# Kernel optimization log

Hardware: AMD Instinct MI355X
Metric: run time of the kernel (lower is better)

The kernel has to match this reference:

```python
import jax, jax.numpy as jnp
import numpy as np

N, D, B, C, T, TOD = 8192, 32, 2, 8, 12, 288
PARAM_SCALE = 0.3  # keep relu+softmax logits well-conditioned (original uses plain randn init)


def setup_inputs() -> dict:
    key = jax.random.key(0)
    k0, k1, k2, k3, k4 = jax.random.split(key, 5)
    return {
        "x": jax.random.normal(k0, (B, C, N, T), dtype=jnp.float32),
        "nodevec1": PARAM_SCALE * jax.random.normal(k1, (N, D), dtype=jnp.float32),
        "nodevec2": PARAM_SCALE * jax.random.normal(k2, (N, D), dtype=jnp.float32),
        "timevec": PARAM_SCALE * jax.random.normal(k3, (TOD, D), dtype=jnp.float32),
        "k": PARAM_SCALE * jax.random.normal(k4, (D, D, D), dtype=jnp.float32),
        "time_ind": 100,
    }


def reference(x, nodevec1, nodevec2, timevec, k, time_ind):
    # Dynamic Tucker-decomposition adjacency (SpatialGraphConv.forward, eval mode -> dropout is identity)
    tv = timevec[time_ind]                             # [D]   time_vec
    core = jnp.einsum('d,def->ef', tv, k)              # [D,D] adp1 (squeezed)
    # adp2/adp3 chain: (nodevec1 @ core) @ nodevec2.T  -> [N,N]
    adp = jnp.einsum('ne,ef->nf', nodevec1, core)      # [N,D]
    adp = jnp.einsum('nf,mf->nm', adp, nodevec2)       # [N,N]
    adp = jax.nn.softmax(jax.nn.relu(adp), axis=-1)    # row-softmax over neighbors
    # NConv: neighbor aggregation  'bcnt,nm->bcmt'
    return jnp.einsum('bcnt,nm->bcmt', x, adp)
```

## Files before the change

### kernel.cpp

```cpp
#include <hip/hip_runtime.h>
#include <hip/hip_bf16.h>


#define NN 8192
#define DD 32
#define TT 12
#define NSPLIT 8
#define CHUNK 1024
#define ESTR 72

typedef __attribute__((ext_vector_type(8))) short bf16x8;
typedef __attribute__((ext_vector_type(4))) short bf16x4;
typedef __attribute__((ext_vector_type(4))) float f32x4;

static __device__ __forceinline__ unsigned short f2bf(float f) {
  unsigned int u = __float_as_uint(f);
  u = (u + 0x7FFFu + ((u >> 16) & 1u)) >> 16;
  return (unsigned short)u;
}

static __device__ __forceinline__ float fexp2(float x) {
#if __has_builtin(__builtin_amdgcn_exp2f)
  return __builtin_amdgcn_exp2f(x);
#else
  return __builtin_exp2f(x);
#endif
}

__global__ __launch_bounds__(256) void k_prep(const float* __restrict__ nv1,
                                              const float* __restrict__ nv2,
                                              const float* __restrict__ timevec,
                                              const float* __restrict__ kk,
                                              const int* __restrict__ tind,
                                              unsigned short* __restrict__ t1b,
                                              unsigned short* __restrict__ nv2b,
                                              float* __restrict__ sums) {
  __shared__ float cs[1024];
  const int tid = threadIdx.x;
  if (tid < 128) sums[blockIdx.x * 128 + tid] = 0.f;
  const float* tv = timevec + (size_t)tind[0] * DD;
  for (int idx = tid; idx < 1024; idx += 256) {
    float acc = 0.f;
#pragma unroll
    for (int d = 0; d < DD; ++d) acc += tv[d] * kk[d * 1024 + idx];
    cs[idx] = acc;
  }
  __syncthreads();
  const int nbase = blockIdx.x * 128;
  const int f = tid & 31, sub = tid >> 5;
#pragma unroll 4
  for (int it = 0; it < 16; ++it) {
    const int n = nbase + it * 8 + sub;
    const float* nr = nv1 + (size_t)n * DD;
    float acc = 0.f;
#pragma unroll
    for (int e = 0; e < DD; ++e) acc += nr[e] * cs[e * DD + f];
    t1b[(size_t)n * DD + f] = f2bf(acc * 1.4426950408889634f);
  }
#pragma unroll 4
  for (int it = 0; it < 16; ++it) {
    const int idx = nbase * DD + it * 256 + tid;
    nv2b[idx] = f2bf(nv2[idx]);
  }
}

__global__ __launch_bounds__(256) void k_stats(const unsigned short* __restrict__ t1b,
                                               const unsigned short* __restrict__ nv2b,
                                               float* __restrict__ sums) {
  const int tid = threadIdx.x;
  const int w = tid >> 6, lane = tid & 63, q = lane >> 4, i16 = lane & 15;
  const int nbase = blockIdx.x * 64 + w * 16;
  bf16x8 a = *(const bf16x8*)(t1b + (size_t)(nbase + i16) * DD + q * 8);
  const f32x4 z4 = {0.f, 0.f, 0.f, 0.f};
  float s[4] = {0.f, 0.f, 0.f, 0.f};
  const int m0 = blockIdx.y * 1024;
  for (int mt = m0; mt < m0 + 1024; mt += 64) {
#pragma unroll
    for (int u = 0; u < 4; ++u) {
      bf16x8 b = *(const bf16x8*)(nv2b + (size_t)(mt + u * 16 + i16) * DD + q * 8);
      f32x4 d = __builtin_amdgcn_mfma_f32_16x16x32_bf16(a, b, z4, 0, 0, 0);
#pragma unroll
      for (int r = 0; r < 4; ++r) s[r] += fexp2(fmaxf(d[r], 0.f));
    }
  }
#pragma unroll
  for (int r = 0; r < 4; ++r)
    for (int off = 1; off < 16; off <<= 1) s[r] += __shfl_xor(s[r], off, 64);
  if (i16 == 0) {
#pragma unroll
    for (int r = 0; r < 4; ++r) atomicAdd(&sums[nbase + q * 4 + r], s[r]);
  }
}

__global__ __launch_bounds__(256) void k_y(const float* __restrict__ x,
                                           const float* __restrict__ sums,
                                           unsigned short* __restrict__ yT) {
  __shared__ float xs[3072];
  const int tid = threadIdx.x;
  const int n0 = blockIdx.x * 256;
  const int bc = blockIdx.y;
  const float* xp = x + (size_t)bc * NN * TT + (size_t)n0 * TT;
#pragma unroll
  for (int j = 0; j < 12; ++j) xs[j * 256 + tid] = xp[j * 256 + tid];
  __syncthreads();
  const float rinv = 1.0f / sums[n0 + tid];
#pragma unroll
  for (int t = 0; t < 12; ++t)
    yT[(size_t)(bc * TT + t) * NN + n0 + tid] = f2bf(xs[tid * 12 + t] * rinv);
}

__global__ __launch_bounds__(256, 4) void k_mega(const unsigned short* __restrict__ t1b,
                                                 const unsigned short* __restrict__ nv2b,
                                                 const unsigned short* __restrict__ yT,
                                                 float* __restrict__ part) {
  const int tid = threadIdx.x;
  const int w = tid >> 6, lane = tid & 63, q = lane >> 4, i16 = lane & 15;
  const int mb = blockIdx.x * 64;
  const int nt0 = blockIdx.y * CHUNK;

  __shared__ unsigned short Ew[2][64][ESTR];

  const bf16x8 bg = *(const bf16x8*)(nv2b + (size_t)(mb + w * 16 + i16) * DD + q * 8);
  const int rowm = w * 16 + i16;

  const f32x4 z4 = {0.f, 0.f, 0.f, 0.f};
  f32x4 acc[3][4];
#pragma unroll
  for (int c = 0; c < 3; ++c)
#pragma unroll
    for (int ms = 0; ms < 4; ++ms) acc[c][ms] = (f32x4){0.f, 0.f, 0.f, 0.f};

#pragma unroll
  for (int s = 0; s < 4; ++s) {
    bf16x8 at = *(const bf16x8*)(t1b + (size_t)(nt0 + s * 16 + i16) * DD + q * 8);
    f32x4 d = __builtin_amdgcn_mfma_f32_16x16x32_bf16(at, bg, z4, 0, 0, 0);
    bf16x4 e;
#pragma unroll
    for (int r = 0; r < 4; ++r) e[r] = (short)f2bf(fexp2(fmaxf(d[r], 0.f)));
    *(bf16x4*)&Ew[0][rowm][s * 16 + q * 4] = e;
  }
  __syncthreads();

  int p = 0;
  for (int st = 0; st < 16; ++st, p ^= 1) {
    const int nt = nt0 + st * 64;
    const bool more = (st < 15);

    bf16x8 atn[4];
    if (more) {
#pragma unroll
      for (int s = 0; s < 4; ++s)
        atn[s] = *(const bf16x8*)(t1b + (size_t)(nt + 64 + s * 16 + i16) * DD + q * 8);
    }

    bf16x8 yfr[3], efr[4];
#pragma unroll
    for (int c = 0; c < 3; ++c)
      yfr[c] = *(const bf16x8*)(yT + (size_t)((w * 3 + c) * 16 + i16) * NN + nt + q * 8);
#pragma unroll
    for (int ms = 0; ms < 4; ++ms)
      efr[ms] = *(const bf16x8*)&Ew[p][ms * 16 + i16][q * 8];

    f32x4 d0, d1;
    if (more) {
      d0 = __builtin_amdgcn_mfma_f32_16x16x32_bf16(atn[0], bg, z4, 0, 0, 0);
      d1 = __builtin_amdgcn_mfma_f32_16x16x32_bf16(atn[1], bg, z4, 0, 0, 0);
    }

#pragma unroll
    for (int c = 0; c < 3; ++c)
#pragma unroll
      for (int ms = 0; ms < 4; ++ms)
        acc[c][ms] = __builtin_amdgcn_mfma_f32_16x16x32_bf16(yfr[c], efr[ms], acc[c][ms], 0, 0, 0);

    if (more) {
      bf16x4 e0, e1;
#pragma unroll
      for (int r = 0; r < 4; ++r) {
        e0[r] = (short)f2bf(fexp2(fmaxf(d0[r], 0.f)));
        e1[r] = (short)f2bf(fexp2(fmaxf(d1[r], 0.f)));
      }
      *(bf16x4*)&Ew[p ^ 1][rowm][q * 4] = e0;
      *(bf16x4*)&Ew[p ^ 1][rowm][16 + q * 4] = e1;
      f32x4 d2 = __builtin_amdgcn_mfma_f32_16x16x32_bf16(atn[2], bg, z4, 0, 0, 0);
      f32x4 d3 = __builtin_amdgcn_mfma_f32_16x16x32_bf16(atn[3], bg, z4, 0, 0, 0);
      bf16x4 e2, e3;
#pragma unroll
      for (int r = 0; r < 4; ++r) {
        e2[r] = (short)f2bf(fexp2(fmaxf(d2[r], 0.f)));
        e3[r] = (short)f2bf(fexp2(fmaxf(d3[r], 0.f)));
      }
      *(bf16x4*)&Ew[p ^ 1][rowm][32 + q * 4] = e2;
      *(bf16x4*)&Ew[p ^ 1][rowm][48 + q * 4] = e3;
    }

#pragma unroll
    for (int c = 0; c < 3; ++c)
      yfr[c] = *(const bf16x8*)(yT + (size_t)((w * 3 + c) * 16 + i16) * NN + nt + 32 + q * 8);
#pragma unroll
    for (int ms = 0; ms < 4; ++ms)
      efr[ms] = *(const bf16x8*)&Ew[p][ms * 16 + i16][32 + q * 8];
#pragma unroll
    for (int c = 0; c < 3; ++c)
#pragma unroll
      for (int ms = 0; ms < 4; ++ms)
        acc[c][ms] = __builtin_amdgcn_mfma_f32_16x16x32_bf16(yfr[c], efr[ms], acc[c][ms], 0, 0, 0);

    __syncthreads();
  }

  float* pp = part + (size_t)blockIdx.y * 192 * NN;
#pragma unroll
  for (int c = 0; c < 3; ++c)
#pragma unroll
    for (int ms = 0; ms < 4; ++ms) {
      const int colbase = (w * 3 + c) * 16 + q * 4;
      const int m = mb + ms * 16 + i16;
#pragma unroll
      for (int r = 0; r < 4; ++r)
        pp[(size_t)(colbase + r) * NN + m] = acc[c][ms][r];
    }
}

__global__ __launch_bounds__(256) void k_reduce(const float* __restrict__ part,
                                                float* __restrict__ out) {
  __shared__ float os[3072];
  const int tid = threadIdx.x;
  const int m0 = blockIdx.x * 256;
  const int bc = blockIdx.y;
#pragma unroll
  for (int t = 0; t < 12; ++t) {
    const int col = bc * TT + t;
    float s = 0.f;
#pragma unroll
    for (int nc = 0; nc < NSPLIT; ++nc)
      s += part[((size_t)nc * 192 + col) * NN + m0 + tid];
    os[tid * 12 + t] = s;
  }
  __syncthreads();
  float* op = out + (size_t)bc * NN * TT + (size_t)m0 * TT;
#pragma unroll
  for (int j = 0; j < 12; ++j) op[j * 256 + tid] = os[j * 256 + tid];
}

extern "C" void kernel_launch(void* const* d_in, const int* in_sizes, int n_in,
                              void* d_out, int out_size, void* d_ws, size_t ws_size,
                              hipStream_t stream) {
  const float* x = (const float*)d_in[0];
  const float* nv1 = (const float*)d_in[1];
  const float* nv2 = (const float*)d_in[2];
  const float* tv = (const float*)d_in[3];
  const float* kk = (const float*)d_in[4];
  const int* tind = (const int*)d_in[5];
  float* out = (float*)d_out;

  char* ws = (char*)d_ws;
  unsigned short* t1b  = (unsigned short*)(ws);
  unsigned short* nv2b = (unsigned short*)(ws + 524288);
  float* sums          = (float*)(ws + 1048576);
  unsigned short* yT   = (unsigned short*)(ws + 1081344);
  float* part          = (float*)(ws + 4227072);

  k_prep<<<64, 256, 0, stream>>>(nv1, nv2, tv, kk, tind, t1b, nv2b, sums);
  k_stats<<<dim3(128, 8), 256, 0, stream>>>(t1b, nv2b, sums);
  k_y<<<dim3(32, 16), 256, 0, stream>>>(x, sums, yT);
  k_mega<<<dim3(128, NSPLIT), 256, 0, stream>>>(t1b, nv2b, yT, part);
  k_reduce<<<dim3(32, 16), 256, 0, stream>>>(part, out);
}
```

Measured before the change: 178.8 us.

## Switch aggregation GEMM to 32x32x16 MFMA with two-stage t1 prefetch

The main aggregation GEMM moves from 16x16x32 to 32x32x16 bf16 MFMA, and the four waves are split as a 2x2 grid over output columns and m rows, which changes fragment loads and the output write pattern. Loads of the next t1 tile are issued two stages ahead and carried in registers, so the exp tile computation no longer waits on a global load issued in the same iteration. The larger MFMA tiles mean fewer LDS and global fragment loads per FLOP. The cost is more live registers, so launch bounds drop from 4 to 3 blocks per CU, which may reduce occupancy.

```diff
diff --git a/kernel.cpp b/kernel.cpp
--- a/kernel.cpp
+++ b/kernel.cpp
@@ -12,6 +12,7 @@
 typedef __attribute__((ext_vector_type(8))) short bf16x8;
 typedef __attribute__((ext_vector_type(4))) short bf16x4;
 typedef __attribute__((ext_vector_type(4))) float f32x4;
+typedef __attribute__((ext_vector_type(16))) float f32x16;
 
 static __device__ __forceinline__ unsigned short f2bf(float f) {
   unsigned int u = __float_as_uint(f);
@@ -109,12 +110,14 @@
     yT[(size_t)(bc * TT + t) * NN + n0 + tid] = f2bf(xs[tid * 12 + t] * rinv);
 }
 
-__global__ __launch_bounds__(256, 4) void k_mega(const unsigned short* __restrict__ t1b,
+__global__ __launch_bounds__(256, 3) void k_mega(const unsigned short* __restrict__ t1b,
                                                  const unsigned short* __restrict__ nv2b,
                                                  const unsigned short* __restrict__ yT,
                                                  float* __restrict__ part) {
   const int tid = threadIdx.x;
   const int w = tid >> 6, lane = tid & 63, q = lane >> 4, i16 = lane & 15;
+  const int h = lane >> 5, l31 = lane & 31;
+  const int wc = w & 1, wm = w >> 1;
   const int mb = blockIdx.x * 64;
   const int nt0 = blockIdx.y * CHUNK;
 
@@ -124,11 +127,11 @@
   const int rowm = w * 16 + i16;
 
   const f32x4 z4 = {0.f, 0.f, 0.f, 0.f};
-  f32x4 acc[3][4];
+  f32x16 acc[3];
 #pragma unroll
   for (int c = 0; c < 3; ++c)
 #pragma unroll
-    for (int ms = 0; ms < 4; ++ms) acc[c][ms] = (f32x4){0.f, 0.f, 0.f, 0.f};
+    for (int r = 0; r < 16; ++r) acc[c][r] = 0.f;
 
 #pragma unroll
   for (int s = 0; s < 4; ++s) {
@@ -139,6 +142,10 @@
     for (int r = 0; r < 4; ++r) e[r] = (short)f2bf(fexp2(fmaxf(d[r], 0.f)));
     *(bf16x4*)&Ew[0][rowm][s * 16 + q * 4] = e;
   }
+  bf16x8 atc[4];
+#pragma unroll
+  for (int s = 0; s < 4; ++s)
+    atc[s] = *(const bf16x8*)(t1b + (size_t)(nt0 + 64 + s * 16 + i16) * DD + q * 8);
   __syncthreads();
 
   int p = 0;
@@ -147,65 +154,47 @@
     const bool more = (st < 15);
 
     bf16x8 atn[4];
+    if (st < 14) {
+#pragma unroll
+      for (int s = 0; s < 4; ++s)
+        atn[s] = *(const bf16x8*)(t1b + (size_t)(nt + 128 + s * 16 + i16) * DD + q * 8);
+    }
+
+    bf16x8 yf[3][4];
+#pragma unroll
+    for (int c = 0; c < 3; ++c) {
+      const unsigned short* yp = yT + (size_t)((wc * 3 + c) * 32 + l31) * NN + nt + h * 8;
+#pragma unroll
+      for (int ks = 0; ks < 4; ++ks) yf[c][ks] = *(const bf16x8*)(yp + ks * 16);
+    }
+
+    bf16x8 ef[4];
+#pragma unroll
+    for (int ks = 0; ks < 4; ++ks)
+      ef[ks] = *(const bf16x8*)&Ew[p][wm * 32 + l31][ks * 16 + h * 8];
+
+    f32x4 dg[4];
     if (more) {
 #pragma unroll
       for (int s = 0; s < 4; ++s)
-        atn[s] = *(const bf16x8*)(t1b + (size_t)(nt + 64 + s * 16 + i16) * DD + q * 8);
-    }
-
-    bf16x8 yfr[3], efr[4];
-#pragma unroll
-    for (int c = 0; c < 3; ++c)
-      yfr[c] = *(const bf16x8*)(yT + (size_t)((w * 3 + c) * 16 + i16) * NN + nt + q * 8);
-#pragma unroll
-    for (int ms = 0; ms < 4; ++ms)
-      efr[ms] = *(const bf16x8*)&Ew[p][ms * 16 + i16][q * 8];
-
-    f32x4 d0, d1;
-    if (more) {
-      d0 = __builtin_amdgcn_mfma_f32_16x16x32_bf16(atn[0], bg, z4, 0, 0, 0);
-      d1 = __builtin_amdgcn_mfma_f32_16x16x32_bf16(atn[1], bg, z4, 0, 0, 0);
-    }
-
-#pragma unroll
-    for (int c = 0; c < 3; ++c)
-#pragma unroll
-      for (int ms = 0; ms < 4; ++ms)
-        acc[c][ms] = __builtin_amdgcn_mfma_f32_16x16x32_bf16(yfr[c], efr[ms], acc[c][ms], 0, 0, 0);
-
-    if (more) {
-      bf16x4 e0, e1;
-#pragma unroll
-      for (int r = 0; r < 4; ++r) {
-        e0[r] = (short)f2bf(fexp2(fmaxf(d0[r], 0.f)));
-        e1[r] = (short)f2bf(fexp2(fmaxf(d1[r], 0.f)));
+        dg[s] = __builtin_amdgcn_mfma_f32_16x16x32_bf16(atc[s], bg, z4, 0, 0, 0);
+#pragma unroll
+      for (int s = 0; s < 4; ++s) {
+        bf16x4 e;
+#pragma unroll
+        for (int r = 0; r < 4; ++r) e[r] = (short)f2bf(fexp2(fmaxf(dg[s][r], 0.f)));
+        *(bf16x4*)&Ew[p ^ 1][rowm][s * 16 + q * 4] = e;
       }
-      *(bf16x4*)&Ew[p ^ 1][rowm][q * 4] = e0;
-      *(bf16x4*)&Ew[p ^ 1][rowm][16 + q * 4] = e1;
-      f32x4 d2 = __builtin_amdgcn_mfma_f32_16x16x32_bf16(atn[2], bg, z4, 0, 0, 0);
-      f32x4 d3 = __builtin_amdgcn_mfma_f32_16x16x32_bf16(atn[3], bg, z4, 0, 0, 0);
-      bf16x4 e2, e3;
-#pragma unroll
-      for (int r = 0; r < 4; ++r) {
-        e2[r] = (short)f2bf(fexp2(fmaxf(d2[r], 0.f)));
-        e3[r] = (short)f2bf(fexp2(fmaxf(d3[r], 0.f)));
-      }
-      *(bf16x4*)&Ew[p ^ 1][rowm][32 + q * 4] = e2;
-      *(bf16x4*)&Ew[p ^ 1][rowm][48 + q * 4] = e3;
-    }
-
-#pragma unroll
-    for (int c = 0; c < 3; ++c)
-      yfr[c] = *(const bf16x8*)(yT + (size_t)((w * 3 + c) * 16 + i16) * NN + nt + 32 + q * 8);
-#pragma unroll
-    for (int ms = 0; ms < 4; ++ms)
-      efr[ms] = *(const bf16x8*)&Ew[p][ms * 16 + i16][32 + q * 8];
-#pragma unroll
-    for (int c = 0; c < 3; ++c)
-#pragma unroll
-      for (int ms = 0; ms < 4; ++ms)
-        acc[c][ms] = __builtin_amdgcn_mfma_f32_16x16x32_bf16(yfr[c], efr[ms], acc[c][ms], 0, 0, 0);
-
+    }
+
+#pragma unroll
+    for (int ks = 0; ks < 4; ++ks)
+#pragma unroll
+      for (int c = 0; c < 3; ++c)
+        acc[c] = __builtin_amdgcn_mfma_f32_32x32x16_bf16(yf[c][ks], ef[ks], acc[c], 0, 0, 0);
+
+#pragma unroll
+    for (int s = 0; s < 4; ++s) atc[s] = atn[s];
     __syncthreads();
   }
 
@@ -213,12 +202,9 @@
 #pragma unroll
   for (int c = 0; c < 3; ++c)
 #pragma unroll
-    for (int ms = 0; ms < 4; ++ms) {
-      const int colbase = (w * 3 + c) * 16 + q * 4;
-      const int m = mb + ms * 16 + i16;
-#pragma unroll
-      for (int r = 0; r < 4; ++r)
-        pp[(size_t)(colbase + r) * NN + m] = acc[c][ms][r];
+    for (int r = 0; r < 16; ++r) {
+      const int col = (wc * 3 + c) * 32 + (r & 3) + 8 * (r >> 2) + 4 * h;
+      pp[(size_t)col * NN + mb + wm * 32 + l31] = acc[c][r];
     }
 }
 
```

After: 217.8 us. 21.8% more time.

## Precompute whole exp-adjacency chunk into large LDS before the aggregation GEMM

Applied to the files above, without the earlier changes.

The main kernel now runs in two phases. First it computes the full 64x1024 tile of exp(relu(logits)) for its chunk and stores it in about 131 KB of dynamic LDS. Then it runs the aggregation MFMA loop with no per-step barriers or interleaved exp work, which removes the double-buffer synchronisation. The cost is that occupancy drops to one block per CU and the exp phase no longer overlaps with the GEMM. If the device reports too little shared memory per block, the launcher falls back to the old double-buffered kernel.

```diff
diff --git a/kernel.cpp b/kernel.cpp
--- a/kernel.cpp
+++ b/kernel.cpp
@@ -8,6 +8,8 @@
 #define NSPLIT 8
 #define CHUNK 1024
 #define ESTR 72
+#define ESTR2 1048
+#define MEGA_LDS (64 * ESTR2 * 2)
 
 typedef __attribute__((ext_vector_type(8))) short bf16x8;
 typedef __attribute__((ext_vector_type(4))) short bf16x4;
@@ -109,27 +111,101 @@
     yT[(size_t)(bc * TT + t) * NN + n0 + tid] = f2bf(xs[tid * 12 + t] * rinv);
 }
 
-__global__ __launch_bounds__(256, 4) void k_mega(const unsigned short* __restrict__ t1b,
+__global__ __launch_bounds__(256, 1) void k_mega(const unsigned short* __restrict__ t1b,
                                                  const unsigned short* __restrict__ nv2b,
                                                  const unsigned short* __restrict__ yT,
                                                  float* __restrict__ part) {
+  extern __shared__ unsigned short Et[];
   const int tid = threadIdx.x;
   const int w = tid >> 6, lane = tid & 63, q = lane >> 4, i16 = lane & 15;
   const int mb = blockIdx.x * 64;
   const int nt0 = blockIdx.y * CHUNK;
-
+  const f32x4 z4 = {0.f, 0.f, 0.f, 0.f};
+
+  {
+    const bf16x8 bg = *(const bf16x8*)(nv2b + (size_t)(mb + w * 16 + i16) * DD + q * 8);
+    unsigned short* erow = Et + (size_t)(w * 16 + i16) * ESTR2;
+    bf16x8 at[4], nx[4];
+#pragma unroll
+    for (int s = 0; s < 4; ++s)
+      at[s] = *(const bf16x8*)(t1b + (size_t)(nt0 + s * 16 + i16) * DD + q * 8);
+    for (int g = 0; g < 16; ++g) {
+      if (g < 15) {
+#pragma unroll
+        for (int s = 0; s < 4; ++s)
+          nx[s] = *(const bf16x8*)(t1b + (size_t)(nt0 + (g + 1) * 64 + s * 16 + i16) * DD + q * 8);
+      }
+#pragma unroll
+      for (int s = 0; s < 4; ++s) {
+        f32x4 d = __builtin_amdgcn_mfma_f32_16x16x32_bf16(at[s], bg, z4, 0, 0, 0);
+        bf16x4 e;
+#pragma unroll
+        for (int r = 0; r < 4; ++r) e[r] = (short)f2bf(fexp2(fmaxf(d[r], 0.f)));
+        *(bf16x4*)&erow[g * 64 + s * 16 + q * 4] = e;
+      }
+#pragma unroll
+      for (int s = 0; s < 4; ++s) at[s] = nx[s];
+    }
+  }
+  __syncthreads();
+
+  f32x4 acc[3][4];
+#pragma unroll
+  for (int c = 0; c < 3; ++c)
+#pragma unroll
+    for (int ms = 0; ms < 4; ++ms) acc[c][ms] = (f32x4){0.f, 0.f, 0.f, 0.f};
+
+  const unsigned short* yp[3];
+#pragma unroll
+  for (int c = 0; c < 3; ++c)
+    yp[c] = yT + (size_t)((w * 3 + c) * 16 + i16) * NN + nt0 + q * 8;
+
+#pragma unroll 2
+  for (int st = 0; st < 32; ++st) {
+    const int nb = st * 32;
+    bf16x8 yfr[3], efr[4];
+#pragma unroll
+    for (int c = 0; c < 3; ++c) yfr[c] = *(const bf16x8*)(yp[c] + nb);
+#pragma unroll
+    for (int ms = 0; ms < 4; ++ms)
+      efr[ms] = *(const bf16x8*)&Et[(size_t)(ms * 16 + i16) * ESTR2 + nb + q * 8];
+#pragma unroll
+    for (int c = 0; c < 3; ++c)
+#pragma unroll
+      for (int ms = 0; ms < 4; ++ms)
+        acc[c][ms] = __builtin_amdgcn_mfma_f32_16x16x32_bf16(yfr[c], efr[ms], acc[c][ms], 0, 0, 0);
+  }
+
+  float* pp = part + (size_t)blockIdx.y * 192 * NN;
+#pragma unroll
+  for (int c = 0; c < 3; ++c)
+#pragma unroll
+    for (int ms = 0; ms < 4; ++ms) {
+      const int colbase = (w * 3 + c) * 16 + q * 4;
+      const int m = mb + ms * 16 + i16;
+#pragma unroll
+      for (int r = 0; r < 4; ++r)
+        pp[(size_t)(colbase + r) * NN + m] = acc[c][ms][r];
+    }
+}
+
+__global__ __launch_bounds__(256, 4) void k_mega_fb(const unsigned short* __restrict__ t1b,
+                                                    const unsigned short* __restrict__ nv2b,
+                                                    const unsigned short* __restrict__ yT,
+                                                    float* __restrict__ part) {
+  const int tid = threadIdx.x;
+  const int w = tid >> 6, lane = tid & 63, q = lane >> 4, i16 = lane & 15;
+  const int mb = blockIdx.x * 64;
+  const int nt0 = blockIdx.y * CHUNK;
   __shared__ unsigned short Ew[2][64][ESTR];
-
   const bf16x8 bg = *(const bf16x8*)(nv2b + (size_t)(mb + w * 16 + i16) * DD + q * 8);
   const int rowm = w * 16 + i16;
-
   const f32x4 z4 = {0.f, 0.f, 0.f, 0.f};
   f32x4 acc[3][4];
 #pragma unroll
   for (int c = 0; c < 3; ++c)
 #pragma unroll
     for (int ms = 0; ms < 4; ++ms) acc[c][ms] = (f32x4){0.f, 0.f, 0.f, 0.f};
-
 #pragma unroll
   for (int s = 0; s < 4; ++s) {
     bf16x8 at = *(const bf16x8*)(t1b + (size_t)(nt0 + s * 16 + i16) * DD + q * 8);
@@ -140,19 +216,16 @@
     *(bf16x4*)&Ew[0][rowm][s * 16 + q * 4] = e;
   }
   __syncthreads();
-
   int p = 0;
   for (int st = 0; st < 16; ++st, p ^= 1) {
     const int nt = nt0 + st * 64;
     const bool more = (st < 15);
-
     bf16x8 atn[4];
     if (more) {
 #pragma unroll
       for (int s = 0; s < 4; ++s)
         atn[s] = *(const bf16x8*)(t1b + (size_t)(nt + 64 + s * 16 + i16) * DD + q * 8);
     }
-
     bf16x8 yfr[3], efr[4];
 #pragma unroll
     for (int c = 0; c < 3; ++c)
@@ -160,19 +233,16 @@
 #pragma unroll
     for (int ms = 0; ms < 4; ++ms)
       efr[ms] = *(const bf16x8*)&Ew[p][ms * 16 + i16][q * 8];
-
     f32x4 d0, d1;
     if (more) {
       d0 = __builtin_amdgcn_mfma_f32_16x16x32_bf16(atn[0], bg, z4, 0, 0, 0);
       d1 = __builtin_amdgcn_mfma_f32_16x16x32_bf16(atn[1], bg, z4, 0, 0, 0);
     }
-
 #pragma unroll
     for (int c = 0; c < 3; ++c)
 #pragma unroll
       for (int ms = 0; ms < 4; ++ms)
         acc[c][ms] = __builtin_amdgcn_mfma_f32_16x16x32_bf16(yfr[c], efr[ms], acc[c][ms], 0, 0, 0);
-
     if (more) {
       bf16x4 e0, e1;
 #pragma unroll
@@ -193,7 +263,6 @@
       *(bf16x4*)&Ew[p ^ 1][rowm][32 + q * 4] = e2;
       *(bf16x4*)&Ew[p ^ 1][rowm][48 + q * 4] = e3;
     }
-
 #pragma unroll
     for (int c = 0; c < 3; ++c)
       yfr[c] = *(const bf16x8*)(yT + (size_t)((w * 3 + c) * 16 + i16) * NN + nt + 32 + q * 8);
@@ -205,10 +274,8 @@
 #pragma unroll
       for (int ms = 0; ms < 4; ++ms)
         acc[c][ms] = __builtin_amdgcn_mfma_f32_16x16x32_bf16(yfr[c], efr[ms], acc[c][ms], 0, 0, 0);
-
     __syncthreads();
   }
-
   float* pp = part + (size_t)blockIdx.y * 192 * NN;
 #pragma unroll
   for (int c = 0; c < 3; ++c)
@@ -264,6 +331,17 @@
   k_prep<<<64, 256, 0, stream>>>(nv1, nv2, tv, kk, tind, t1b, nv2b, sums);
   k_stats<<<dim3(128, 8), 256, 0, stream>>>(t1b, nv2b, sums);
   k_y<<<dim3(32, 16), 256, 0, stream>>>(x, sums, yT);
-  k_mega<<<dim3(128, NSPLIT), 256, 0, stream>>>(t1b, nv2b, yT, part);
+
+  int dev = 0;
+  (void)hipGetDevice(&dev);
+  int maxshm = 0;
+  (void)hipDeviceGetAttribute(&maxshm, hipDeviceAttributeMaxSharedMemoryPerBlock, dev);
+  (void)hipFuncSetAttribute((const void*)k_mega, hipFuncAttributeMaxDynamicSharedMemorySize,
+                            MEGA_LDS);
+  if (maxshm >= MEGA_LDS) {
+    k_mega<<<dim3(128, NSPLIT), 256, MEGA_LDS, stream>>>(t1b, nv2b, yT, part);
+  } else {
+    k_mega_fb<<<dim3(128, NSPLIT), 256, 0, stream>>>(t1b, nv2b, yT, part);
+  }
   k_reduce<<<dim3(32, 16), 256, 0, stream>>>(part, out);
 }
```

New measurement: 188.7 us. +5.5%, slower.
